# Performance work log

Measured on AMD Instinct MI355X. Metric: run time of the kernel, lower is better.

## Reference

```python
import jax, jax.numpy as jnp
import numpy as np

SEQ, B, IN, H, OUT, L = 256, 64, 512, 1024, 256, 2
DT = 0.05

def setup_inputs() -> dict:
    key = jax.random.key(0)
    ks = jax.random.split(key, 10)
    s = lambda fan_in: 1.0 / np.sqrt(fan_in)
    return {
        "x":    jax.random.normal(ks[0], (SEQ, B, IN), dtype=jnp.float32),
        "W_in": jax.random.uniform(ks[1], (H, IN), jnp.float32, -s(IN), s(IN)),
        "b_in": jax.random.uniform(ks[2], (H,), jnp.float32, -s(IN), s(IN)),
        "W_c":  jax.random.uniform(ks[3], (H, 2 * H), jnp.float32, -s(2 * H), s(2 * H)),
        "b_c":  jax.random.uniform(ks[4], (H,), jnp.float32, -s(2 * H), s(2 * H)),
        "taus": jnp.ones((L,), jnp.float32),
        "W_o1": jax.random.uniform(ks[5], (H // 2, H), jnp.float32, -s(H), s(H)),
        "b_o1": jax.random.uniform(ks[6], (H // 2,), jnp.float32, -s(H), s(H)),
        "W_o2": jax.random.uniform(ks[7], (OUT, H // 2), jnp.float32, -s(H // 2), s(H // 2)),
        "b_o2": jax.random.uniform(ks[8], (OUT,), jnp.float32, -s(H // 2), s(H // 2)),
    }

def reference(x, W_in, b_in, W_c, b_c, taus, W_o1, b_o1, W_o2, b_o2):
    # input projection for all timesteps at once: [S,B,IN] -> [S,B,H]
    xp = jnp.einsum('sbi,hi->sbh', x, W_in) + b_in
    num_layers = taus.shape[0]
    batch = x.shape[1]
    hidden0 = jnp.zeros((num_layers, batch, W_in.shape[0]), dtype=x.dtype)

    def step(hidden, xt):
        inp = xt  # [B,H]
        new_hidden = []
        for layer in range(num_layers):
            h = hidden[layer]
            # original code calls cell(input_t.detach(), h): stop gradient on input path
            comb = jnp.concatenate([jax.lax.stop_gradient(inp), h], axis=-1)  # [B,2H]
            dhdt = jnp.tanh(comb @ W_c.T + b_c)
            h_next = h + (DT / (taus[layer] + 0.001)) * dhdt
            new_hidden.append(h_next)
            inp = h_next
        hidden = jnp.stack(new_hidden)  # [L,B,H]
        out = jax.nn.relu(hidden[-1] @ W_o1.T + b_o1) @ W_o2.T + b_o2  # [B,OUT]
        return hidden, out

    hidden_final, outputs = jax.lax.scan(step, hidden0, xp)
    return outputs, hidden_final
```

## Files before the change

kernel.cpp:

```cpp
#include <hip/hip_runtime.h>
#include <hip/hip_bf16.h>
#include <stdint.h>

typedef unsigned short ushort_t;
typedef unsigned long long ull_t;
using bf16x8 = __attribute__((ext_vector_type(8))) short;
using f32x4  = __attribute__((ext_vector_type(4))) float;

#define SEQ    256
#define BATCH  64
#define INDIM  512
#define HDIM   1024
#define OUTDIM 256
#define MTOT   (SEQ*BATCH)
#define BH     (BATCH*HDIM)
#define WPAD   1032

__device__ __forceinline__ ushort_t f2bf(float f) {
  uint32_t u = __builtin_bit_cast(uint32_t, f);
  u += 0x7fffu + ((u >> 16) & 1u);
  return (ushort_t)(u >> 16);
}
__device__ __forceinline__ float bf2f(ushort_t b) {
  uint32_t u = ((uint32_t)b) << 16;
  return __builtin_bit_cast(float, u);
}
__device__ __forceinline__ f32x4 mfma16(bf16x8 a, bf16x8 b, f32x4 c) {
  return __builtin_amdgcn_mfma_f32_16x16x32_bf16(a, b, c, 0, 0, 0);
}
__device__ __forceinline__ void gload16(const void* g, void* l) {
  __builtin_amdgcn_global_load_lds(
      (const __attribute__((address_space(1))) unsigned int*)g,
      (__attribute__((address_space(3))) unsigned int*)l, 16, 0, 0);
}
__device__ __forceinline__ float tanhfast(float z) {
  float e = __expf(2.0f * z);
  return 1.0f - 2.0f / (e + 1.0f);
}
__device__ __forceinline__ int load_sc0_int(const int* p) {
  int v;
  asm volatile("global_load_dword %0, %1, off sc0\n\ts_waitcnt vmcnt(0)"
               : "=&v"(v) : "v"(p) : "memory");
  return v;
}

__global__ void k_convert(const float* __restrict__ src, ushort_t* __restrict__ dst, int n) {
  int i = blockIdx.x * blockDim.x + threadIdx.x;
  if (i < n) dst[i] = f2bf(src[i]);
}
__global__ void k_split(const float* __restrict__ src, ushort_t* __restrict__ hi,
                        ushort_t* __restrict__ lo, int n) {
  int i = blockIdx.x * blockDim.x + threadIdx.x;
  if (i < n) {
    float v = src[i];
    ushort_t h = f2bf(v);
    hi[i] = h;
    lo[i] = f2bf(v - bf2f(h));
  }
}
__global__ void k_split_wc(const float* __restrict__ Wc,
                           ushort_t* __restrict__ WiH, ushort_t* __restrict__ WiL,
                           ushort_t* __restrict__ WhH, ushort_t* __restrict__ WhL) {
  int i = blockIdx.x * blockDim.x + threadIdx.x;
  if (i < HDIM * HDIM) {
    int row = i >> 10, k = i & 1023;
    float vi = Wc[(size_t)row * (2 * HDIM) + k];
    float vh = Wc[(size_t)row * (2 * HDIM) + HDIM + k];
    ushort_t ih = f2bf(vi);
    WiH[i] = ih; WiL[i] = f2bf(vi - bf2f(ih));
    ushort_t hh = f2bf(vh);
    WhH[i] = hh; WhL[i] = f2bf(vh - bf2f(hh));
  }
}

template<int SPLITB, int RELU, int OUTBF>
__global__ __launch_bounds__(256) void gemm_nt(
    const ushort_t* __restrict__ A, const ushort_t* __restrict__ Bhi,
    const ushort_t* __restrict__ Blo, const float* __restrict__ bias,
    float* __restrict__ Cf, ushort_t* __restrict__ Cb,
    int M, int N, int K)
{
  __shared__ ushort_t As[128 * 32];
  __shared__ ushort_t Bh[128 * 32];
  __shared__ ushort_t Bl[128 * 32];
  const int tid = threadIdx.x;
  const int w = tid >> 6, l = tid & 63;
  const int m0 = blockIdx.x * 128, n0 = blockIdx.y * 128;
  const int wr = w >> 1, wc = w & 1;
  const int lr = l & 15, lk = l >> 4;

  f32x4 acc[4][4] = {};
  const int nK = K >> 5;
  const size_t rowB = (size_t)K * 2;

  for (int kk = 0; kk < nK; ++kk) {
    const size_t kbyte = (size_t)kk * 64;
#pragma unroll
    for (int j = 0; j < 2; ++j) {
      int c = (w * 2 + j) * 64 + l;
      int row = c >> 2;
      int kb = (c & 3) * 16;
      gload16((const char*)A + (size_t)(m0 + row) * rowB + kbyte + kb,
              (char*)As + (w * 2 + j) * 1024);
      gload16((const char*)Bhi + (size_t)(n0 + row) * rowB + kbyte + kb,
              (char*)Bh + (w * 2 + j) * 1024);
      if (SPLITB)
        gload16((const char*)Blo + (size_t)(n0 + row) * rowB + kbyte + kb,
                (char*)Bl + (w * 2 + j) * 1024);
    }
    __syncthreads();
    bf16x8 af[4], bhf[4], blf[4];
#pragma unroll
    for (int i = 0; i < 4; ++i) {
      af[i]  = *(const bf16x8*)&As[(wr * 64 + i * 16 + lr) * 32 + lk * 8];
      bhf[i] = *(const bf16x8*)&Bh[(wc * 64 + i * 16 + lr) * 32 + lk * 8];
      if (SPLITB)
        blf[i] = *(const bf16x8*)&Bl[(wc * 64 + i * 16 + lr) * 32 + lk * 8];
    }
#pragma unroll
    for (int i = 0; i < 4; ++i)
#pragma unroll
      for (int j2 = 0; j2 < 4; ++j2) {
        acc[i][j2] = mfma16(af[i], bhf[j2], acc[i][j2]);
        if (SPLITB) acc[i][j2] = mfma16(af[i], blf[j2], acc[i][j2]);
      }
    __syncthreads();
  }
#pragma unroll
  for (int j2 = 0; j2 < 4; ++j2) {
    int n = n0 + wc * 64 + j2 * 16 + lr;
    float bv = bias ? bias[n] : 0.0f;
#pragma unroll
    for (int i = 0; i < 4; ++i) {
#pragma unroll
      for (int r = 0; r < 4; ++r) {
        int m = m0 + wr * 64 + i * 16 + lk * 4 + r;
        float v = acc[i][j2][r] + bv;
        if (RELU) v = fmaxf(v, 0.0f);
        if (OUTBF) Cb[(size_t)m * N + n] = f2bf(v);
        else       Cf[(size_t)m * N + n] = v;
      }
    }
  }
}

__global__ __attribute__((amdgpu_waves_per_eu(2, 2))) __launch_bounds__(512)
void scan_kernel(
    const float* __restrict__ P0,
    const ushort_t* __restrict__ WiH, const ushort_t* __restrict__ WiL,
    const ushort_t* __restrict__ WhH, const ushort_t* __restrict__ WhL,
    const float* __restrict__ b_c, const float* __restrict__ taus,
    ushort_t* __restrict__ h0buf,
    ushort_t* __restrict__ H1buf,
    float* __restrict__ outHidden, int* __restrict__ sync)
{
  __shared__ float red[4 * 8 * 320];
  __shared__ ushort_t WhLds[32 * WPAD];
  __shared__ int meta[2];

  const int tid = threadIdx.x;
  const int w = tid >> 6, l = tid & 63;
  const int lr = l & 15, lk = l >> 4;

  int* cnt        = sync;
  int* flags_l2   = sync + 64;
  int* flags_mall = sync + 192;

  if (tid == 0) {
    int xcd;
    asm volatile("s_getreg_b32 %0, hwreg(HW_REG_XCC_ID)" : "=s"(xcd));
    int slot = 999;
    if (xcd < 4)
      slot = __hip_atomic_fetch_add(&cnt[xcd], 1, __ATOMIC_RELAXED,
                                    __HIP_MEMORY_SCOPE_AGENT);
    meta[0] = (xcd < 4) ? xcd : -1;
    meta[1] = slot;
  }
  __syncthreads();
  const int g = meta[0];
  const int c = meta[1];
  if (g < 0 || c >= 32) return;

  const int rowg = g * 16, colg = c * 32;
  const int kb = w * 128;

  {
    const ushort_t* wsrc = WhH + (size_t)colg * HDIM;
#pragma unroll
    for (int j = 0; j < 8; ++j) {
      int e = (j * 512 + tid) * 8;
      bf16x8 v = *(const bf16x8*)&wsrc[e];
      *(bf16x8*)&WhLds[(e >> 10) * WPAD + (e & 1023)] = v;
    }
  }
  bf16x8 wl[2][4], wi[2][4];
#pragma unroll
  for (int ct = 0; ct < 2; ++ct)
#pragma unroll
    for (int kk = 0; kk < 4; ++kk) {
      size_t off = (size_t)(colg + ct * 16 + lr) * HDIM + kb + kk * 32 + lk * 8;
      wl[ct][kk] = *(const bf16x8*)&WhL[off];
      wi[ct][kk] = *(const bf16x8*)&WiH[off];
    }
  __syncthreads();

  const int ep = (w < 4);
  const int ph = w >> 1, ect = w & 1;
  const int ec = lr, R0 = lk * 4;
  float hm[4] = {0, 0, 0, 0};
  float bcn = 0.f, alpha = 0.f;
  float p0r[4] = {0, 0, 0, 0};
  if (ep) {
    alpha = 0.05f / (taus[ph] + 0.001f);
    bcn = b_c[colg + ect * 16 + ec];
    if (ph == 0) {
#pragma unroll
      for (int j = 0; j < 4; ++j)
        p0r[j] = P0[((size_t)0 * BATCH + rowg + R0 + j) * HDIM + colg + ect * 16 + ec];
    }
  }

  for (int i = 0; i <= SEQ; ++i) {
#pragma unroll
    for (int ct = 0; ct < 2; ++ct)
#pragma unroll
      for (int kk = 0; kk < 4; ++kk)
        asm volatile("" : "+v"(wl[ct][kk]), "+v"(wi[ct][kk]));

    bf16x8 f[4] = {}, hh[4] = {};
    f32x4 aA[2] = {}, aI[2] = {}, aH[2] = {};
    if (i >= 1) {
      const ushort_t* h0r = h0buf + (size_t)(i - 1) * BH;
#pragma unroll
      for (int kk = 0; kk < 4; ++kk)
        f[kk] = *(const bf16x8*)&h0r[(size_t)(rowg + lr) * HDIM + kb + kk * 32 + lk * 8];
      if (i >= 2) {
        const ushort_t* h1r = H1buf + (size_t)(i - 2) * BH;
#pragma unroll
        for (int kk = 0; kk < 4; ++kk)
          hh[kk] = *(const bf16x8*)&h1r[(size_t)(rowg + lr) * HDIM + kb + kk * 32 + lk * 8];
      }
#pragma unroll
      for (int ct = 0; ct < 2; ++ct)
#pragma unroll
        for (int kk = 0; kk < 4; ++kk) {
          bf16x8 wh = *(const bf16x8*)&WhLds[(ct * 16 + lr) * WPAD + kb + kk * 32 + lk * 8];
          aA[ct] = mfma16(f[kk], wh, aA[ct]);
          aA[ct] = mfma16(f[kk], wl[ct][kk], aA[ct]);
          aI[ct] = mfma16(f[kk], wi[ct][kk], aI[ct]);
          if (i >= 2) {
            aH[ct] = mfma16(hh[kk], wh, aH[ct]);
            aH[ct] = mfma16(hh[kk], wl[ct][kk], aH[ct]);
          }
        }
    }
    const int wbase = lr * 20 + lk * 4;
#pragma unroll
    for (int ct = 0; ct < 2; ++ct) {
      *(f32x4*)&red[((0 + ct) * 8 + w) * 320 + wbase] = aA[ct];
      f32x4 pb = aI[ct] + aH[ct];
      *(f32x4*)&red[((2 + ct) * 8 + w) * 320 + wbase] = pb;
    }
    __syncthreads();

    if (ep && ((ph == 0 && i < SEQ) || (ph == 1 && i >= 1))) {
      f32x4 s = {};
      const float* rb = &red[(w * 8) * 320 + ec * 20 + R0];
#pragma unroll
      for (int q = 0; q < 8; ++q)
        s += *(const f32x4*)&rb[q * 320];
      if (ph == 0) {
        ushort_t* dst = &h0buf[(size_t)i * BH + (size_t)(rowg + R0) * HDIM +
                               colg + ect * 16 + ec];
#pragma unroll
        for (int j = 0; j < 4; ++j) {
          hm[j] += alpha * tanhfast(p0r[j] + s[j]);
          dst[(size_t)j * HDIM] = f2bf(hm[j]);
        }
      } else {
        ushort_t* dst = &H1buf[(size_t)(i - 1) * BH + (size_t)(rowg + R0) * HDIM +
                               colg + ect * 16 + ec];
#pragma unroll
        for (int j = 0; j < 4; ++j) {
          hm[j] += alpha * tanhfast(s[j] + bcn);
          dst[(size_t)j * HDIM] = f2bf(hm[j]);
        }
      }
      asm volatile("s_waitcnt vmcnt(0)" ::: "memory");
    }
    __syncthreads();

    if (i < SEQ) {
      if (tid == 0) {
        *(volatile int*)&flags_l2[g * 32 + c] = i + 1;
        asm volatile("" ::: "memory");
        __hip_atomic_store(&flags_mall[g * 32 + c], i + 1, __ATOMIC_RELAXED,
                           __HIP_MEMORY_SCOPE_AGENT);
      }
      if (ep && ph == 0 && i + 1 < SEQ) {
#pragma unroll
        for (int j = 0; j < 4; ++j)
          p0r[j] = P0[((size_t)(i + 1) * BATCH + rowg + R0 + j) * HDIM +
                      colg + ect * 16 + ec];
      }
      if (w == 4) {
        const int target = i + 1;
        const int* fl2 = &flags_l2[g * 32 + (l & 31)];
        int* fml = &flags_mall[g * 32 + (l & 31)];
        for (int r = 0;; ++r) {
          int v = ((r & 3) == 3)
            ? __hip_atomic_load(fml, __ATOMIC_RELAXED, __HIP_MEMORY_SCOPE_AGENT)
            : load_sc0_int(fl2);
          if (__all(v >= target)) break;
        }
      }
      __syncthreads();
    }
  }

  if (ep) {
    float* dst = &outHidden[(size_t)ph * BH + (size_t)(rowg + R0) * HDIM +
                            colg + ect * 16 + ec];
#pragma unroll
    for (int j = 0; j < 4; ++j) dst[(size_t)j * HDIM] = hm[j];
  }
}

extern "C" void kernel_launch(void* const* d_in, const int* in_sizes, int n_in,
                              void* d_out, int out_size, void* d_ws, size_t ws_size,
                              hipStream_t stream) {
  const float* x    = (const float*)d_in[0];
  const float* W_in = (const float*)d_in[1];
  const float* b_in = (const float*)d_in[2];
  const float* W_c  = (const float*)d_in[3];
  const float* b_c  = (const float*)d_in[4];
  const float* taus = (const float*)d_in[5];
  const float* W_o1 = (const float*)d_in[6];
  const float* b_o1 = (const float*)d_in[7];
  const float* W_o2 = (const float*)d_in[8];
  const float* b_o2 = (const float*)d_in[9];
  float* out = (float*)d_out;

  char* ws = (char*)d_ws;
  size_t off = 0;
  auto alloc = [&](size_t bytes) -> char* {
    char* p = ws + off;
    off += (bytes + 255) & ~(size_t)255;
    return p;
  };
  ushort_t* x_bf  = (ushort_t*)alloc((size_t)MTOT * INDIM * 2);
  ushort_t* xp_b  = (ushort_t*)alloc((size_t)MTOT * HDIM * 2);
  float*    P0    = (float*)   alloc((size_t)MTOT * HDIM * 4);
  ushort_t* H1buf = (ushort_t*)alloc((size_t)MTOT * HDIM * 2);
  ushort_t* h0buf = (ushort_t*)alloc((size_t)SEQ * BH * 2);
  ushort_t* O1    = (ushort_t*)alloc((size_t)MTOT * (HDIM/2) * 2);
  ushort_t* WiH   = (ushort_t*)alloc((size_t)HDIM * HDIM * 2);
  ushort_t* WiL   = (ushort_t*)alloc((size_t)HDIM * HDIM * 2);
  ushort_t* WhH   = (ushort_t*)alloc((size_t)HDIM * HDIM * 2);
  ushort_t* WhL   = (ushort_t*)alloc((size_t)HDIM * HDIM * 2);
  ushort_t* WinH  = (ushort_t*)alloc((size_t)HDIM * INDIM * 2);
  ushort_t* WinL  = (ushort_t*)alloc((size_t)HDIM * INDIM * 2);
  ushort_t* Wo1b  = (ushort_t*)alloc((size_t)(HDIM/2) * HDIM * 2);
  ushort_t* Wo2b  = (ushort_t*)alloc((size_t)OUTDIM * (HDIM/2) * 2);
  int*      sync  = (int*)     alloc(4096);
  if (off > ws_size) return;

  hipMemsetAsync(sync, 0, 4096, stream);

  k_convert<<<(MTOT * INDIM + 255) / 256, 256, 0, stream>>>(x, x_bf, MTOT * INDIM);
  k_split<<<(HDIM * INDIM + 255) / 256, 256, 0, stream>>>(W_in, WinH, WinL, HDIM * INDIM);
  k_split_wc<<<(HDIM * HDIM + 255) / 256, 256, 0, stream>>>(W_c, WiH, WiL, WhH, WhL);
  k_convert<<<((HDIM/2) * HDIM + 255) / 256, 256, 0, stream>>>(W_o1, Wo1b, (HDIM/2) * HDIM);
  k_convert<<<(OUTDIM * (HDIM/2) + 255) / 256, 256, 0, stream>>>(W_o2, Wo2b, OUTDIM * (HDIM/2));

  gemm_nt<1, 0, 1><<<dim3(MTOT / 128, HDIM / 128), 256, 0, stream>>>(
      x_bf, WinH, WinL, b_in, nullptr, xp_b, MTOT, HDIM, INDIM);
  gemm_nt<1, 0, 0><<<dim3(MTOT / 128, HDIM / 128), 256, 0, stream>>>(
      xp_b, WiH, WiL, b_c, P0, nullptr, MTOT, HDIM, HDIM);

  scan_kernel<<<512, 512, 0, stream>>>(P0, WiH, WiL, WhH, WhL, b_c, taus,
                                       h0buf, H1buf,
                                       out + (size_t)SEQ * BATCH * OUTDIM, sync);

  gemm_nt<0, 1, 1><<<dim3(MTOT / 128, (HDIM/2) / 128), 256, 0, stream>>>(
      H1buf, Wo1b, nullptr, b_o1, nullptr, O1, MTOT, HDIM / 2, HDIM);
  gemm_nt<0, 0, 0><<<dim3(MTOT / 128, OUTDIM / 128), 256, 0, stream>>>(
      O1, Wo2b, nullptr, b_o2, out, nullptr, MTOT, OUTDIM, HDIM / 2);
}
```

Baseline: 1.290 ms.

## Decentralize scan step barrier with per-wave flag polling and double-buffered reduction

Replaces the block-wide barrier plus single-wave spin wait with a scheme where each wave polls only the four producer flags its K-slice depends on, at the start of the next step. Completion flags are published by the last epilogue wave through an LDS counter, so no trailing __syncthreads is needed. The reduction buffer is double-buffered with a padded stride to avoid races and bank conflicts. Flags are padded to separate cache lines. The intent is to shorten the per-step critical path of the recurrent scan. The cost is more polling traffic and more delicate memory-ordering assumptions.

```diff
diff --git a/kernel.cpp b/kernel.cpp
--- a/kernel.cpp
+++ b/kernel.cpp
@@ -15,6 +15,7 @@
 #define MTOT   (SEQ*BATCH)
 #define BH     (BATCH*HDIM)
 #define WPAD   1032
+#define RSTR   324
 
 __device__ __forceinline__ ushort_t f2bf(float f) {
   uint32_t u = __builtin_bit_cast(uint32_t, f);
@@ -42,6 +43,9 @@
   asm volatile("global_load_dword %0, %1, off sc0\n\ts_waitcnt vmcnt(0)"
                : "=&v"(v) : "v"(p) : "memory");
   return v;
+}
+__device__ __forceinline__ void store_sc0_int(int* p, int v) {
+  asm volatile("global_store_dword %0, %1, off sc0" :: "v"(p), "v"(v) : "memory");
 }
 
 __global__ void k_convert(const float* __restrict__ src, ushort_t* __restrict__ dst, int n) {
@@ -144,6 +148,7 @@
   }
 }
 
+#define RIDX(buf, tile, q) ((((buf)*4 + (tile))*8 + (q)) * RSTR)
 __global__ __attribute__((amdgpu_waves_per_eu(2, 2))) __launch_bounds__(512)
 void scan_kernel(
     const float* __restrict__ P0,
@@ -154,17 +159,18 @@
     ushort_t* __restrict__ H1buf,
     float* __restrict__ outHidden, int* __restrict__ sync)
 {
-  __shared__ float red[4 * 8 * 320];
+  __shared__ float red[2 * 4 * 8 * RSTR];
   __shared__ ushort_t WhLds[32 * WPAD];
   __shared__ int meta[2];
+  __shared__ int dcnt;
 
   const int tid = threadIdx.x;
   const int w = tid >> 6, l = tid & 63;
   const int lr = l & 15, lk = l >> 4;
 
   int* cnt        = sync;
-  int* flags_l2   = sync + 64;
-  int* flags_mall = sync + 192;
+  int* flags_l2   = sync + 256;
+  int* flags_mall = sync + 256 + 2048;
 
   if (tid == 0) {
     int xcd;
@@ -175,6 +181,7 @@
                                     __HIP_MEMORY_SCOPE_AGENT);
     meta[0] = (xcd < 4) ? xcd : -1;
     meta[1] = slot;
+    dcnt = 0;
   }
   __syncthreads();
   const int g = meta[0];
@@ -203,6 +210,9 @@
       wi[ct][kk] = *(const bf16x8*)&WiH[off];
     }
   __syncthreads();
+
+  const int* fl2p = &flags_l2[(g * 32 + w * 4 + (l & 3)) * 16];
+  int*       fmlp = &flags_mall[(g * 32 + w * 4 + (l & 3)) * 16];
 
   const int ep = (w < 4);
   const int ph = w >> 1, ect = w & 1;
@@ -227,6 +237,18 @@
       for (int kk = 0; kk < 4; ++kk)
         asm volatile("" : "+v"(wl[ct][kk]), "+v"(wi[ct][kk]));
 
+    if (i >= 1) {
+      const int target = i;
+      for (int r = 0;; ++r) {
+        int v = 0x7fffffff;
+        if (l < 4)
+          v = ((r & 7) == 7)
+            ? __hip_atomic_load(fmlp, __ATOMIC_RELAXED, __HIP_MEMORY_SCOPE_AGENT)
+            : load_sc0_int(fl2p);
+        if (__all(v >= target)) break;
+      }
+    }
+
     bf16x8 f[4] = {}, hh[4] = {};
     f32x4 aA[2] = {}, aI[2] = {}, aH[2] = {};
     if (i >= 1) {
@@ -254,67 +276,58 @@
           }
         }
     }
+    const int buf = i & 1;
     const int wbase = lr * 20 + lk * 4;
 #pragma unroll
     for (int ct = 0; ct < 2; ++ct) {
-      *(f32x4*)&red[((0 + ct) * 8 + w) * 320 + wbase] = aA[ct];
+      *(f32x4*)&red[RIDX(buf, ct, w) + wbase] = aA[ct];
       f32x4 pb = aI[ct] + aH[ct];
-      *(f32x4*)&red[((2 + ct) * 8 + w) * 320 + wbase] = pb;
+      *(f32x4*)&red[RIDX(buf, 2 + ct, w) + wbase] = pb;
     }
     __syncthreads();
 
-    if (ep && ((ph == 0 && i < SEQ) || (ph == 1 && i >= 1))) {
-      f32x4 s = {};
-      const float* rb = &red[(w * 8) * 320 + ec * 20 + R0];
-#pragma unroll
-      for (int q = 0; q < 8; ++q)
-        s += *(const f32x4*)&rb[q * 320];
-      if (ph == 0) {
-        ushort_t* dst = &h0buf[(size_t)i * BH + (size_t)(rowg + R0) * HDIM +
-                               colg + ect * 16 + ec];
-#pragma unroll
-        for (int j = 0; j < 4; ++j) {
-          hm[j] += alpha * tanhfast(p0r[j] + s[j]);
-          dst[(size_t)j * HDIM] = f2bf(hm[j]);
+    if (ep) {
+      const bool act = (ph == 0 && i < SEQ) || (ph == 1 && i >= 1);
+      if (act) {
+        f32x4 s = {};
+        const float* rb = &red[RIDX(buf, w, 0) + ec * 20 + R0];
+#pragma unroll
+        for (int q = 0; q < 8; ++q)
+          s += *(const f32x4*)&rb[q * RSTR];
+        if (ph == 0) {
+          ushort_t* dst = &h0buf[(size_t)i * BH + (size_t)(rowg + R0) * HDIM +
+                                 colg + ect * 16 + ec];
+#pragma unroll
+          for (int j = 0; j < 4; ++j) {
+            hm[j] += alpha * tanhfast(p0r[j] + s[j]);
+            dst[(size_t)j * HDIM] = f2bf(hm[j]);
+          }
+        } else {
+          ushort_t* dst = &H1buf[(size_t)(i - 1) * BH + (size_t)(rowg + R0) * HDIM +
+                                 colg + ect * 16 + ec];
+#pragma unroll
+          for (int j = 0; j < 4; ++j) {
+            hm[j] += alpha * tanhfast(s[j] + bcn);
+            dst[(size_t)j * HDIM] = f2bf(hm[j]);
+          }
         }
-      } else {
-        ushort_t* dst = &H1buf[(size_t)(i - 1) * BH + (size_t)(rowg + R0) * HDIM +
-                               colg + ect * 16 + ec];
-#pragma unroll
-        for (int j = 0; j < 4; ++j) {
-          hm[j] += alpha * tanhfast(s[j] + bcn);
-          dst[(size_t)j * HDIM] = f2bf(hm[j]);
+      }
+      asm volatile("s_waitcnt vmcnt(0)" ::: "memory");
+      if (i < SEQ && l == 0) {
+        int old = __hip_atomic_fetch_add(&dcnt, 1, __ATOMIC_ACQ_REL,
+                                         __HIP_MEMORY_SCOPE_WORKGROUP);
+        if (old == 4 * i + 3) {
+          store_sc0_int(&flags_l2[(g * 32 + c) * 16], i + 1);
+          __hip_atomic_store(&flags_mall[(g * 32 + c) * 16], i + 1,
+                             __ATOMIC_RELAXED, __HIP_MEMORY_SCOPE_AGENT);
         }
       }
-      asm volatile("s_waitcnt vmcnt(0)" ::: "memory");
-    }
-    __syncthreads();
-
-    if (i < SEQ) {
-      if (tid == 0) {
-        *(volatile int*)&flags_l2[g * 32 + c] = i + 1;
-        asm volatile("" ::: "memory");
-        __hip_atomic_store(&flags_mall[g * 32 + c], i + 1, __ATOMIC_RELAXED,
-                           __HIP_MEMORY_SCOPE_AGENT);
-      }
-      if (ep && ph == 0 && i + 1 < SEQ) {
+      if (ph == 0 && i + 1 < SEQ) {
 #pragma unroll
         for (int j = 0; j < 4; ++j)
           p0r[j] = P0[((size_t)(i + 1) * BATCH + rowg + R0 + j) * HDIM +
                       colg + ect * 16 + ec];
       }
-      if (w == 4) {
-        const int target = i + 1;
-        const int* fl2 = &flags_l2[g * 32 + (l & 31)];
-        int* fml = &flags_mall[g * 32 + (l & 31)];
-        for (int r = 0;; ++r) {
-          int v = ((r & 3) == 3)
-            ? __hip_atomic_load(fml, __ATOMIC_RELAXED, __HIP_MEMORY_SCOPE_AGENT)
-            : load_sc0_int(fl2);
-          if (__all(v >= target)) break;
-        }
-      }
-      __syncthreads();
     }
   }
 
@@ -362,10 +375,10 @@
   ushort_t* WinL  = (ushort_t*)alloc((size_t)HDIM * INDIM * 2);
   ushort_t* Wo1b  = (ushort_t*)alloc((size_t)(HDIM/2) * HDIM * 2);
   ushort_t* Wo2b  = (ushort_t*)alloc((size_t)OUTDIM * (HDIM/2) * 2);
-  int*      sync  = (int*)     alloc(4096);
+  int*      sync  = (int*)     alloc(32768);
   if (off > ws_size) return;
 
-  hipMemsetAsync(sync, 0, 4096, stream);
+  hipMemsetAsync(sync, 0, 32768, stream);
 
   k_convert<<<(MTOT * INDIM + 255) / 256, 256, 0, stream>>>(x, x_bf, MTOT * INDIM);
   k_split<<<(HDIM * INDIM + 255) / 256, 256, 0, stream>>>(W_in, WinH, WinL, HDIM * INDIM);
```

Result: no change. 1.275 ms (-1.2%).

## Split per-block step flag into per-layer flags and drop one block barrier per step

Applied to the files above, without the earlier changes.

The single per-block progress flag is replaced by separate layer-0 and layer-1 flags. The epilogue waves publish each flag themselves through a workgroup-shared counter, so the extra __syncthreads before signalling goes away and each step needs one block barrier instead of two. Flags are padded to separate cache lines, the epilogue runs at raised wave priority, and the poller sleeps after a few failed tries. This is meant to shorten the critical path of the cross-block recurrence barrier. In exchange it adds LDS atomics and more complex memory-ordering reasoning, with a risk of subtle visibility bugs.

```diff
diff --git a/kernel.cpp b/kernel.cpp
--- a/kernel.cpp
+++ b/kernel.cpp
@@ -42,6 +42,9 @@
   asm volatile("global_load_dword %0, %1, off sc0\n\ts_waitcnt vmcnt(0)"
                : "=&v"(v) : "v"(p) : "memory");
   return v;
+}
+__device__ __forceinline__ void store_sc0_int(int* p, int v) {
+  asm volatile("global_store_dword %0, %1, off sc0" :: "v"(p), "v"(v) : "memory");
 }
 
 __global__ void k_convert(const float* __restrict__ src, ushort_t* __restrict__ dst, int n) {
@@ -157,14 +160,17 @@
   __shared__ float red[4 * 8 * 320];
   __shared__ ushort_t WhLds[32 * WPAD];
   __shared__ int meta[2];
+  __shared__ int acnt, bcnt;
 
   const int tid = threadIdx.x;
   const int w = tid >> 6, l = tid & 63;
   const int lr = l & 15, lk = l >> 4;
 
-  int* cnt        = sync;
-  int* flags_l2   = sync + 64;
-  int* flags_mall = sync + 192;
+  int* cnt    = sync;
+  int* A_l2   = sync + 256;
+  int* A_mall = sync + 256 + 4096;
+  int* B_l2   = sync + 256 + 8192;
+  int* B_mall = sync + 256 + 12288;
 
   if (tid == 0) {
     int xcd;
@@ -175,6 +181,7 @@
                                     __HIP_MEMORY_SCOPE_AGENT);
     meta[0] = (xcd < 4) ? xcd : -1;
     meta[1] = slot;
+    acnt = 0; bcnt = 0;
   }
   __syncthreads();
   const int g = meta[0];
@@ -203,6 +210,10 @@
       wi[ct][kk] = *(const bf16x8*)&WiH[off];
     }
   __syncthreads();
+
+  const int pl = l & 31;
+  const int* fl2p = (l < 32) ? &A_l2[(g * 32 + pl) * 16] : &B_l2[(g * 32 + pl) * 16];
+  int*       fmlp = (l < 32) ? &A_mall[(g * 32 + pl) * 16] : &B_mall[(g * 32 + pl) * 16];
 
   const int ep = (w < 4);
   const int ph = w >> 1, ect = w & 1;
@@ -263,59 +274,71 @@
     }
     __syncthreads();
 
-    if (ep && ((ph == 0 && i < SEQ) || (ph == 1 && i >= 1))) {
-      f32x4 s = {};
-      const float* rb = &red[(w * 8) * 320 + ec * 20 + R0];
-#pragma unroll
-      for (int q = 0; q < 8; ++q)
-        s += *(const f32x4*)&rb[q * 320];
-      if (ph == 0) {
-        ushort_t* dst = &h0buf[(size_t)i * BH + (size_t)(rowg + R0) * HDIM +
-                               colg + ect * 16 + ec];
-#pragma unroll
-        for (int j = 0; j < 4; ++j) {
-          hm[j] += alpha * tanhfast(p0r[j] + s[j]);
-          dst[(size_t)j * HDIM] = f2bf(hm[j]);
+    if (ep) {
+      const bool act = (ph == 0) ? (i < SEQ) : (i >= 1);
+      if (act) {
+        __builtin_amdgcn_s_setprio(1);
+        f32x4 s = {};
+        const float* rb = &red[(w * 8) * 320 + ec * 20 + R0];
+#pragma unroll
+        for (int q = 0; q < 8; ++q)
+          s += *(const f32x4*)&rb[q * 320];
+        if (ph == 0) {
+          ushort_t* dst = &h0buf[(size_t)i * BH + (size_t)(rowg + R0) * HDIM +
+                                 colg + ect * 16 + ec];
+#pragma unroll
+          for (int j = 0; j < 4; ++j) {
+            hm[j] += alpha * tanhfast(p0r[j] + s[j]);
+            dst[(size_t)j * HDIM] = f2bf(hm[j]);
+          }
+        } else {
+          ushort_t* dst = &H1buf[(size_t)(i - 1) * BH + (size_t)(rowg + R0) * HDIM +
+                                 colg + ect * 16 + ec];
+#pragma unroll
+          for (int j = 0; j < 4; ++j) {
+            hm[j] += alpha * tanhfast(s[j] + bcn);
+            dst[(size_t)j * HDIM] = f2bf(hm[j]);
+          }
         }
-      } else {
-        ushort_t* dst = &H1buf[(size_t)(i - 1) * BH + (size_t)(rowg + R0) * HDIM +
-                               colg + ect * 16 + ec];
-#pragma unroll
-        for (int j = 0; j < 4; ++j) {
-          hm[j] += alpha * tanhfast(s[j] + bcn);
-          dst[(size_t)j * HDIM] = f2bf(hm[j]);
+        asm volatile("s_waitcnt vmcnt(0)" ::: "memory");
+        if (l == 0) {
+          if (ph == 0) {
+            int old = __hip_atomic_fetch_add(&acnt, 1, __ATOMIC_ACQ_REL,
+                                             __HIP_MEMORY_SCOPE_WORKGROUP);
+            if (old == 2 * i + 1) {
+              store_sc0_int(&A_l2[(g * 32 + c) * 16], i + 1);
+              __hip_atomic_store(&A_mall[(g * 32 + c) * 16], i + 1,
+                                 __ATOMIC_RELAXED, __HIP_MEMORY_SCOPE_AGENT);
+            }
+          } else {
+            int old = __hip_atomic_fetch_add(&bcnt, 1, __ATOMIC_ACQ_REL,
+                                             __HIP_MEMORY_SCOPE_WORKGROUP);
+            if (old == 2 * (i - 1) + 1) {
+              store_sc0_int(&B_l2[(g * 32 + c) * 16], i);
+              __hip_atomic_store(&B_mall[(g * 32 + c) * 16], i,
+                                 __ATOMIC_RELAXED, __HIP_MEMORY_SCOPE_AGENT);
+            }
+          }
         }
-      }
-      asm volatile("s_waitcnt vmcnt(0)" ::: "memory");
-    }
-    __syncthreads();
-
-    if (i < SEQ) {
-      if (tid == 0) {
-        *(volatile int*)&flags_l2[g * 32 + c] = i + 1;
-        asm volatile("" ::: "memory");
-        __hip_atomic_store(&flags_mall[g * 32 + c], i + 1, __ATOMIC_RELAXED,
-                           __HIP_MEMORY_SCOPE_AGENT);
-      }
-      if (ep && ph == 0 && i + 1 < SEQ) {
+        __builtin_amdgcn_s_setprio(0);
+      }
+      if (ph == 0 && i + 1 < SEQ) {
 #pragma unroll
         for (int j = 0; j < 4; ++j)
           p0r[j] = P0[((size_t)(i + 1) * BATCH + rowg + R0 + j) * HDIM +
                       colg + ect * 16 + ec];
       }
-      if (w == 4) {
-        const int target = i + 1;
-        const int* fl2 = &flags_l2[g * 32 + (l & 31)];
-        int* fml = &flags_mall[g * 32 + (l & 31)];
-        for (int r = 0;; ++r) {
-          int v = ((r & 3) == 3)
-            ? __hip_atomic_load(fml, __ATOMIC_RELAXED, __HIP_MEMORY_SCOPE_AGENT)
-            : load_sc0_int(fl2);
-          if (__all(v >= target)) break;
-        }
-      }
-      __syncthreads();
-    }
+    } else if (w == 4 && i < SEQ) {
+      const int tgt = (l < 32) ? (i + 1) : i;
+      for (int r = 0;; ++r) {
+        int v = ((r & 15) == 15)
+          ? __hip_atomic_load(fmlp, __ATOMIC_RELAXED, __HIP_MEMORY_SCOPE_AGENT)
+          : load_sc0_int(fl2p);
+        if (__all(v >= tgt)) break;
+        if (r >= 4) __builtin_amdgcn_s_sleep(1);
+      }
+    }
+    __syncthreads();
   }
 
   if (ep) {
@@ -362,10 +385,10 @@
   ushort_t* WinL  = (ushort_t*)alloc((size_t)HDIM * INDIM * 2);
   ushort_t* Wo1b  = (ushort_t*)alloc((size_t)(HDIM/2) * HDIM * 2);
   ushort_t* Wo2b  = (ushort_t*)alloc((size_t)OUTDIM * (HDIM/2) * 2);
-  int*      sync  = (int*)     alloc(4096);
+  int*      sync  = (int*)     alloc(65536);
   if (off > ws_size) return;
 
-  hipMemsetAsync(sync, 0, 4096, stream);
+  hipMemsetAsync(sync, 0, 65536, stream);
 
   k_convert<<<(MTOT * INDIM + 255) / 256, 256, 0, stream>>>(x, x_bf, MTOT * INDIM);
   k_split<<<(HDIM * INDIM + 255) / 256, 256, 0, stream>>>(W_in, WinH, WinL, HDIM * INDIM);
```

Result: slower. 1.636 ms (+26.8%).
